# Performance work log

Measured on AMD Instinct MI355X. Metric: run time of the kernel, lower is better.

Reference implementation:

```python
import jax, jax.numpy as jnp
import numpy as np

HEAD_SIZE = 64  # EMBEDDING_SIZE(384) // HEAD_NO(6)

def setup_inputs() -> dict:
    key = jax.random.key(0)
    ks = jax.random.split(key, 6)
    B, T, C, H, D = 256, 256, 384, 6, 64
    s = 0.02
    return {
        "x": jax.random.normal(ks[0], (B, T, C), dtype=jnp.float32),
        "Wq": jax.random.normal(ks[1], (H, C, D), dtype=jnp.float32) * s,
        "Wk": jax.random.normal(ks[2], (H, C, D), dtype=jnp.float32) * s,
        "Wv": jax.random.normal(ks[3], (H, C, D), dtype=jnp.float32) * s,
        "Wproj": jax.random.normal(ks[4], (C, C), dtype=jnp.float32) * s,
        "bproj": jnp.zeros((C,), dtype=jnp.float32),
    }

def reference(x, Wq, Wk, Wv, Wproj, bproj):
    B, T, C = x.shape
    # per-head projections, stacked over heads h: [B, H, T, D]
    q = jnp.einsum('btc,hcd->bhtd', x, Wq)
    k = jnp.einsum('btc,hcd->bhtd', x, Wk)
    v = jnp.einsum('btc,hcd->bhtd', x, Wv)
    scale = 1.0 / jnp.sqrt(jnp.asarray(HEAD_SIZE, dtype=x.dtype))
    # scores [B, H, T, T]; causal mask (masked_fill then /scale == scale then mask, since -inf/scale=-inf)
    scores = jnp.einsum('bhtd,bhsd->bhts', q, k) * scale
    causal = jnp.tril(jnp.ones((T, T), dtype=bool))
    scores = jnp.where(causal, scores, -jnp.inf)
    w = jax.nn.softmax(scores, axis=-1)
    # dropout is identity in eval mode
    out = jnp.einsum('bhts,bhsd->bhtd', w, v)          # [B, H, T, D]
    out = out.transpose(0, 2, 1, 3).reshape(B, T, C)    # concat heads -> [B, T, C]
    return out @ Wproj + bproj
```

## Files before the change

kernel.cpp:

```cpp
#include <hip/hip_runtime.h>
#include <hip/hip_bf16.h>

typedef __bf16 bf16;
typedef unsigned int u32;
typedef __attribute__((ext_vector_type(8))) __bf16 bf16x8;
typedef __attribute__((ext_vector_type(4))) float f32x4;

#define Bsz 256
#define Tsz 256
#define Csz 384
#define Hn  6
#define Dh  64
#define NQKV 1152

#define MFMA16(a, b, c) __builtin_amdgcn_mfma_f32_16x16x32_bf16(a, b, c, 0, 0, 0)

typedef __attribute__((address_space(3))) u32 lds_u32;
typedef __attribute__((address_space(1))) const u32 gbl_u32;
__device__ __forceinline__ void gl2lds16(const void* g, void* l) {
    __builtin_amdgcn_global_load_lds((gbl_u32*)g, (lds_u32*)l, 16, 0, 0);
}

__device__ __forceinline__ float redmax16(float x) {
    x = fmaxf(x, __shfl_xor(x, 1));
    x = fmaxf(x, __shfl_xor(x, 2));
    x = fmaxf(x, __shfl_xor(x, 4));
    x = fmaxf(x, __shfl_xor(x, 8));
    return x;
}
__device__ __forceinline__ float redsum16(float x) {
    x += __shfl_xor(x, 1);
    x += __shfl_xor(x, 2);
    x += __shfl_xor(x, 4);
    x += __shfl_xor(x, 8);
    return x;
}

__global__ __launch_bounds__(256) void convert_x(
    const float* __restrict__ x, bf16* __restrict__ xb)
{
    size_t i = ((size_t)blockIdx.x * 256 + threadIdx.x) * 8;
    float4 f0 = *(const float4*)&x[i];
    float4 f1 = *(const float4*)&x[i + 4];
    bf16x8 o;
    o[0] = (bf16)f0.x; o[1] = (bf16)f0.y; o[2] = (bf16)f0.z; o[3] = (bf16)f0.w;
    o[4] = (bf16)f1.x; o[5] = (bf16)f1.y; o[6] = (bf16)f1.z; o[7] = (bf16)f1.w;
    *(bf16x8*)&xb[i] = o;
}

__global__ __launch_bounds__(384) void prep_w(
    const float* __restrict__ Wq, const float* __restrict__ Wk,
    const float* __restrict__ Wv, const float* __restrict__ Wp,
    bf16* __restrict__ Btqkv, bf16* __restrict__ Bpt)
{
    const int n = blockIdx.x, k = threadIdx.x;
    if (n < NQKV) {
        int wi = n / Csz, rem = n - wi * Csz, h = rem >> 6, d = rem & 63;
        const float* W = wi == 0 ? Wq : (wi == 1 ? Wk : Wv);
        Btqkv[(size_t)n * Csz + k] = (bf16)W[((size_t)h * Csz + k) * Dh + d];
    } else {
        int n2 = n - NQKV;
        Bpt[(size_t)n2 * Csz + k] = (bf16)Wp[(size_t)k * Csz + n2];
    }
}


__device__ __forceinline__ void stage_tile512(
    const char* Ab, const char* Bb, int m0, int n0, int t,
    char* AsB, char* BsB, int tid)
{
    const int srow = tid >> 3;
    const int scs  = ((tid & 7) * 16) ^ ((srow & 7) << 4);
    #pragma unroll
    for (int j = 0; j < 4; ++j)
        gl2lds16(Ab + (size_t)(m0 + j * 64 + srow) * 768 + t * 128 + scs,
                 AsB + j * 8192 + tid * 16);
    #pragma unroll
    for (int j = 0; j < 2; ++j)
        gl2lds16(Bb + (size_t)(n0 + j * 64 + srow) * 768 + t * 128 + scs,
                 BsB + j * 8192 + tid * 16);
}

__device__ __forceinline__ void compute_tile512(
    const char* Ap, const char* Bp,
    int wm4, int wn2, int l4, int quad, f32x4 acc[4][4])
{
    const int cswz = (l4 & 7) << 4;
    bf16x8 bfr[4][2], af[4][2];
    #pragma unroll
    for (int fn = 0; fn < 4; ++fn)
        #pragma unroll
        for (int ks = 0; ks < 2; ++ks)
            bfr[fn][ks] = *(const bf16x8*)(Bp + (wn2 * 64 + fn * 16 + l4) * 128 +
                                           ((ks * 64 + quad * 16) ^ cswz));
    #pragma unroll
    for (int fr = 0; fr < 4; ++fr)
        #pragma unroll
        for (int ks = 0; ks < 2; ++ks)
            af[fr][ks] = *(const bf16x8*)(Ap + (wm4 * 64 + fr * 16 + l4) * 128 +
                                          ((ks * 64 + quad * 16) ^ cswz));
    __builtin_amdgcn_s_setprio(1);
    #pragma unroll
    for (int ks = 0; ks < 2; ++ks)
        #pragma unroll
        for (int fr = 0; fr < 4; ++fr)
            #pragma unroll
            for (int fn = 0; fn < 4; ++fn)
                acc[fr][fn] = MFMA16(af[fr][ks], bfr[fn][ks], acc[fr][fn]);
    __builtin_amdgcn_s_setprio(0);
}

#define GEMM_PIPE8()                                                           \
    stage_tile512(Ab, Bb, m0, n0, 0, As0, Bs0, tid);                           \
    _Pragma("unroll")                                                          \
    for (int t = 0; t < 6; ++t) {                                              \
        if (t < 5) stage_tile512(Ab, Bb, m0, n0, t + 1,                        \
                                 (t & 1) ? As0 : As1, (t & 1) ? Bs0 : Bs1, tid);\
        if (t < 5) { asm volatile("s_waitcnt vmcnt(6)" ::: "memory"); }        \
        else       { asm volatile("s_waitcnt vmcnt(0)" ::: "memory"); }        \
        __builtin_amdgcn_s_barrier();                                          \
        compute_tile512((t & 1) ? As1 : As0, (t & 1) ? Bs1 : Bs0,              \
                        wm4, wn2, l4, quad, acc);                              \
        __builtin_amdgcn_s_barrier();                                          \
    }

__global__ __launch_bounds__(512, 2) void qkv_gemm(
    const bf16* __restrict__ A, const bf16* __restrict__ Bt,
    bf16* __restrict__ q, bf16* __restrict__ k, bf16* __restrict__ v)
{
    __shared__ bf16 As[2][256][64];
    __shared__ bf16 Bs[2][128][64];
    char* As0 = (char*)&As[0][0][0]; char* As1 = (char*)&As[1][0][0];
    char* Bs0 = (char*)&Bs[0][0][0]; char* Bs1 = (char*)&Bs[1][0][0];
    const int tid = threadIdx.x, w = tid >> 6, lane = tid & 63;
    const int l4 = lane & 15, quad = lane >> 4;
    const int wm4 = w >> 1, wn2 = w & 1;

    const int orig = blockIdx.x;
    const int id = (orig & 7) * 288 + (orig >> 3);
    const int mt_ = id / 9, nt_ = id - mt_ * 9;
    const int m0 = mt_ * 256, n0 = nt_ * 128;

    const char* Ab = (const char*)A;
    const char* Bb = (const char*)Bt;
    f32x4 acc[4][4] = {};

    GEMM_PIPE8();

    #pragma unroll
    for (int fn = 0; fn < 4; ++fn) {
        int n = n0 + wn2 * 64 + fn * 16 + l4;
        int wi = n / Csz, rem = n - wi * Csz;
        int h = rem >> 6, d = rem & 63;
        bf16* outp = wi == 0 ? q : (wi == 1 ? k : v);
        #pragma unroll
        for (int fr = 0; fr < 4; ++fr)
            #pragma unroll
            for (int r = 0; r < 4; ++r) {
                int m = m0 + wm4 * 64 + fr * 16 + quad * 4 + r;
                int b = m >> 8, tt = m & 255;
                outp[(((size_t)(b * Hn + h)) * Tsz + tt) * Dh + d] = (bf16)acc[fr][fn][r];
            }
    }
}

__global__ __launch_bounds__(512, 2) void proj_gemm(
    const bf16* __restrict__ A, const bf16* __restrict__ Bt,
    const float* __restrict__ bias, float* __restrict__ out)
{
    __shared__ bf16 As[2][256][64];
    __shared__ bf16 Bs[2][128][64];
    char* As0 = (char*)&As[0][0][0]; char* As1 = (char*)&As[1][0][0];
    char* Bs0 = (char*)&Bs[0][0][0]; char* Bs1 = (char*)&Bs[1][0][0];
    const int tid = threadIdx.x, w = tid >> 6, lane = tid & 63;
    const int l4 = lane & 15, quad = lane >> 4;
    const int wm4 = w >> 1, wn2 = w & 1;

    const int orig = blockIdx.x;
    const int id = (orig & 7) * 96 + (orig >> 3);
    const int mt_ = id / 3, nt_ = id - mt_ * 3;
    const int m0 = mt_ * 256, n0 = nt_ * 128;

    const char* Ab = (const char*)A;
    const char* Bb = (const char*)Bt;
    f32x4 acc[4][4] = {};

    GEMM_PIPE8();

    #pragma unroll
    for (int fn = 0; fn < 4; ++fn) {
        int n = n0 + wn2 * 64 + fn * 16 + l4;
        float bv = bias[n];
        #pragma unroll
        for (int fr = 0; fr < 4; ++fr)
            #pragma unroll
            for (int r = 0; r < 4; ++r) {
                int m = m0 + wm4 * 64 + fr * 16 + quad * 4 + r;
                out[(size_t)m * Csz + n] = acc[fr][fn][r] + bv;
            }
    }
}

__global__ __launch_bounds__(256) void attn_mfma(
    const bf16* __restrict__ q, const bf16* __restrict__ k, const bf16* __restrict__ v,
    bf16* __restrict__ att)
{
    __shared__ bf16 Kl[64][72];
    __shared__ bf16 Vt[64][72];
    __shared__ bf16 Pl[4][16][72];
    const float SCL = 0.18033688f;
    const int tid = threadIdx.x, w = tid >> 6, lane = tid & 63;
    const int l4 = lane & 15, quad = lane >> 4;

    const int orig = blockIdx.x;
    const int blk = (orig & 7) * 768 + (orig >> 3);
    const int bh = blk >> 2, qt = blk & 3;
    const int b = bh / Hn, h = bh % Hn;
    const bf16* qb = q + (size_t)bh * Tsz * Dh;
    const bf16* kb = k + (size_t)bh * Tsz * Dh;
    const bf16* vb = v + (size_t)bh * Tsz * Dh;

    const int trow = qt * 64 + w * 16 + l4;
    const bf16x8 qa0 = *(const bf16x8*)&qb[trow * Dh + quad * 8];
    const bf16x8 qa1 = *(const bf16x8*)&qb[trow * Dh + 32 + quad * 8];

    f32x4 o[4] = {f32x4{0,0,0,0}, f32x4{0,0,0,0}, f32x4{0,0,0,0}, f32x4{0,0,0,0}};
    float mrun[4] = {-3.0e38f, -3.0e38f, -3.0e38f, -3.0e38f};
    float lrun[4] = {0.f, 0.f, 0.f, 0.f};

    for (int kt = 0; kt <= qt; ++kt) {
        #pragma unroll
        for (int it = 0; it < 2; ++it) {
            int idx = it * 256 + tid;
            int s = idx >> 3, d8 = (idx & 7) * 8;
            *(bf16x8*)&Kl[s][d8] = *(const bf16x8*)&kb[(kt * 64 + s) * Dh + d8];
        }
        #pragma unroll
        for (int it = 0; it < 2; ++it) {
            int idx = it * 256 + tid;
            int s = idx & 63, d8 = (idx >> 6) * 8;
            bf16x8 vv = *(const bf16x8*)&vb[(kt * 64 + s) * Dh + d8];
            #pragma unroll
            for (int j = 0; j < 8; ++j) Vt[d8 + j][s] = vv[j];
        }
        __syncthreads();

        f32x4 sc[4] = {f32x4{0,0,0,0}, f32x4{0,0,0,0}, f32x4{0,0,0,0}, f32x4{0,0,0,0}};
        #pragma unroll
        for (int nt = 0; nt < 4; ++nt) {
            bf16x8 b0 = *(const bf16x8*)&Kl[nt * 16 + l4][quad * 8];
            bf16x8 b1 = *(const bf16x8*)&Kl[nt * 16 + l4][32 + quad * 8];
            sc[nt] = MFMA16(qa0, b0, sc[nt]);
            sc[nt] = MFMA16(qa1, b1, sc[nt]);
        }

        float mnew[4], alpha[4];
        #pragma unroll
        for (int r = 0; r < 4; ++r) {
            int tg = qt * 64 + w * 16 + quad * 4 + r;
            float mx = mrun[r];
            #pragma unroll
            for (int nt = 0; nt < 4; ++nt) {
                float sv = sc[nt][r] * SCL;
                int sg = kt * 64 + nt * 16 + l4;
                if (sg > tg) sv = -1.0e30f;
                sc[nt][r] = sv;
                mx = fmaxf(mx, sv);
            }
            mx = redmax16(mx);
            mnew[r] = mx;
            alpha[r] = __builtin_amdgcn_exp2f(mrun[r] - mx);
            mrun[r] = mx;
        }
        #pragma unroll
        for (int r = 0; r < 4; ++r) {
            float sm = 0.f;
            #pragma unroll
            for (int nt = 0; nt < 4; ++nt) {
                float e = __builtin_amdgcn_exp2f(sc[nt][r] - mnew[r]);
                sc[nt][r] = e;
                sm += e;
            }
            sm = redsum16(sm);
            lrun[r] = lrun[r] * alpha[r] + sm;
        }
        #pragma unroll
        for (int nt = 0; nt < 4; ++nt)
            #pragma unroll
            for (int r = 0; r < 4; ++r) o[nt][r] *= alpha[r];

        #pragma unroll
        for (int nt = 0; nt < 4; ++nt)
            #pragma unroll
            for (int r = 0; r < 4; ++r)
                Pl[w][quad * 4 + r][nt * 16 + l4] = (bf16)sc[nt][r];

        bf16x8 pa0 = *(const bf16x8*)&Pl[w][l4][quad * 8];
        bf16x8 pa1 = *(const bf16x8*)&Pl[w][l4][32 + quad * 8];
        #pragma unroll
        for (int nt = 0; nt < 4; ++nt) {
            bf16x8 vb0 = *(const bf16x8*)&Vt[nt * 16 + l4][quad * 8];
            bf16x8 vb1 = *(const bf16x8*)&Vt[nt * 16 + l4][32 + quad * 8];
            o[nt] = MFMA16(pa0, vb0, o[nt]);
            o[nt] = MFMA16(pa1, vb1, o[nt]);
        }
        __syncthreads();
    }

    #pragma unroll
    for (int r = 0; r < 4; ++r) {
        float inv = 1.f / lrun[r];
        int tg = qt * 64 + w * 16 + quad * 4 + r;
        #pragma unroll
        for (int nt = 0; nt < 4; ++nt)
            att[((size_t)(b * Tsz + tg)) * Csz + h * Dh + nt * 16 + l4] =
                (bf16)(o[nt][r] * inv);
    }
}

extern "C" void kernel_launch(void* const* d_in, const int* in_sizes, int n_in,
                              void* d_out, int out_size, void* d_ws, size_t ws_size,
                              hipStream_t stream)
{
    const float* x  = (const float*)d_in[0];
    const float* Wq = (const float*)d_in[1];
    const float* Wk = (const float*)d_in[2];
    const float* Wv = (const float*)d_in[3];
    const float* Wp = (const float*)d_in[4];
    const float* bp = (const float*)d_in[5];
    float* out = (float*)d_out;

    const size_t npe = (size_t)Bsz * Tsz * Csz;
    bf16* xb    = (bf16*)d_ws;
    bf16* att   = xb;
    bf16* q     = xb + npe;
    bf16* k     = q  + npe;
    bf16* v     = k  + npe;
    bf16* Btqkv = v  + npe;
    bf16* Bpt   = Btqkv + (size_t)NQKV * Csz;

    convert_x<<<npe / 2048, 256, 0, stream>>>(x, xb);
    prep_w<<<NQKV + Csz, 384, 0, stream>>>(Wq, Wk, Wv, Wp, Btqkv, Bpt);
    qkv_gemm<<<(Bsz * Tsz / 256) * (NQKV / 128), 512, 0, stream>>>(xb, Btqkv, q, k, v);
    attn_mfma<<<Bsz * Hn * 4, 256, 0, stream>>>(q, k, v, att);
    proj_gemm<<<(Bsz * Tsz / 256) * (Csz / 128), 512, 0, stream>>>(att, Bpt, bp, out);
}
```

Baseline: 388.6 us.

## Restructure attention to one block per (batch, head) with full K/V in LDS

The attention kernel now runs one 512-thread block per (batch, head). It loads all 256 K rows and a transposed V into XOR-swizzled LDS once, so the previous per-query-tile reloads of K/V and the barriers inside the loop are gone. Each wave handles two 16-row query groups chosen as w and 15-w to balance the causal work. Masking is applied only on the diagonal tile, and s_setprio brackets the MFMA sections. The cost is more LDS per block (about 80KB), which limits occupancy, and a smaller grid that may underfill the CUs.

```diff
diff --git a/kernel.cpp b/kernel.cpp
--- a/kernel.cpp
+++ b/kernel.cpp
@@ -201,120 +201,146 @@
     }
 }
 
-__global__ __launch_bounds__(256) void attn_mfma(
+__global__ __launch_bounds__(512, 4) void attn_mfma(
     const bf16* __restrict__ q, const bf16* __restrict__ k, const bf16* __restrict__ v,
     bf16* __restrict__ att)
 {
-    __shared__ bf16 Kl[64][72];
-    __shared__ bf16 Vt[64][72];
-    __shared__ bf16 Pl[4][16][72];
+    __shared__ bf16 Kl[256][64];
+    __shared__ bf16 Vt[64][256];
+    __shared__ bf16 Pl[8][16][64];
     const float SCL = 0.18033688f;
     const int tid = threadIdx.x, w = tid >> 6, lane = tid & 63;
     const int l4 = lane & 15, quad = lane >> 4;
-
-    const int orig = blockIdx.x;
-    const int blk = (orig & 7) * 768 + (orig >> 3);
-    const int bh = blk >> 2, qt = blk & 3;
+    const int cswz = l4 & 7;
+    const int bh = blockIdx.x;
     const int b = bh / Hn, h = bh % Hn;
     const bf16* qb = q + (size_t)bh * Tsz * Dh;
     const bf16* kb = k + (size_t)bh * Tsz * Dh;
     const bf16* vb = v + (size_t)bh * Tsz * Dh;
-
-    const int trow = qt * 64 + w * 16 + l4;
-    const bf16x8 qa0 = *(const bf16x8*)&qb[trow * Dh + quad * 8];
-    const bf16x8 qa1 = *(const bf16x8*)&qb[trow * Dh + 32 + quad * 8];
-
-    f32x4 o[4] = {f32x4{0,0,0,0}, f32x4{0,0,0,0}, f32x4{0,0,0,0}, f32x4{0,0,0,0}};
-    float mrun[4] = {-3.0e38f, -3.0e38f, -3.0e38f, -3.0e38f};
-    float lrun[4] = {0.f, 0.f, 0.f, 0.f};
-
-    for (int kt = 0; kt <= qt; ++kt) {
-        #pragma unroll
-        for (int it = 0; it < 2; ++it) {
-            int idx = it * 256 + tid;
-            int s = idx >> 3, d8 = (idx & 7) * 8;
-            *(bf16x8*)&Kl[s][d8] = *(const bf16x8*)&kb[(kt * 64 + s) * Dh + d8];
+    char* KlB = (char*)&Kl[0][0];
+    char* VtB = (char*)&Vt[0][0];
+    char* PlB = (char*)&Pl[w][0][0];
+
+    bf16x8 qa[2][2];
+    #pragma unroll
+    for (int fi = 0; fi < 2; ++fi) {
+        int g = fi ? 15 - w : w;
+        qa[fi][0] = *(const bf16x8*)&qb[(g * 16 + l4) * Dh + quad * 8];
+        qa[fi][1] = *(const bf16x8*)&qb[(g * 16 + l4) * Dh + 32 + quad * 8];
+    }
+
+    #pragma unroll
+    for (int it = 0; it < 4; ++it) {
+        int c = it * 512 + tid;
+        int row = c >> 3, ck = c & 7;
+        bf16x8 kv = *(const bf16x8*)((const char*)kb + (size_t)c * 16);
+        *(bf16x8*)(KlB + row * 128 + ((ck ^ (row & 7)) << 4)) = kv;
+    }
+    #pragma unroll
+    for (int it = 0; it < 4; ++it) {
+        int idx = it * 512 + tid;
+        int s = idx & 63, g2 = idx >> 6;
+        int d8 = (g2 & 7) * 8, sg = (g2 >> 3) * 64 + s;
+        bf16x8 vv = *(const bf16x8*)&vb[(size_t)sg * Dh + d8];
+        #pragma unroll
+        for (int j = 0; j < 8; ++j) {
+            int row = d8 + j;
+            *(bf16*)(VtB + row * 512 + (((sg >> 3) ^ (row & 7)) << 4) + (sg & 7) * 2) = vv[j];
         }
-        #pragma unroll
-        for (int it = 0; it < 2; ++it) {
-            int idx = it * 256 + tid;
-            int s = idx & 63, d8 = (idx >> 6) * 8;
-            bf16x8 vv = *(const bf16x8*)&vb[(kt * 64 + s) * Dh + d8];
-            #pragma unroll
-            for (int j = 0; j < 8; ++j) Vt[d8 + j][s] = vv[j];
+    }
+    __syncthreads();
+
+    #pragma unroll
+    for (int fi = 0; fi < 2; ++fi) {
+        const int g = fi ? 15 - w : w;
+        const int diag = g >> 2;
+        const int tg = g * 16 + quad * 4;
+        f32x4 o[4] = {f32x4{0,0,0,0}, f32x4{0,0,0,0}, f32x4{0,0,0,0}, f32x4{0,0,0,0}};
+        float mrun[4] = {-3.0e38f, -3.0e38f, -3.0e38f, -3.0e38f};
+        float lrun[4] = {0.f, 0.f, 0.f, 0.f};
+
+        for (int kt = 0; kt <= diag; ++kt) {
+            f32x4 sc[4] = {f32x4{0,0,0,0}, f32x4{0,0,0,0}, f32x4{0,0,0,0}, f32x4{0,0,0,0}};
+            __builtin_amdgcn_s_setprio(1);
+            #pragma unroll
+            for (int nt = 0; nt < 4; ++nt) {
+                const char* kbase = KlB + (kt * 64 + nt * 16 + l4) * 128;
+                bf16x8 b0 = *(const bf16x8*)(kbase + ((quad ^ cswz) << 4));
+                bf16x8 b1 = *(const bf16x8*)(kbase + (((4 + quad) ^ cswz) << 4));
+                sc[nt] = MFMA16(qa[fi][0], b0, sc[nt]);
+                sc[nt] = MFMA16(qa[fi][1], b1, sc[nt]);
+            }
+            __builtin_amdgcn_s_setprio(0);
+
+            const bool isdiag = (kt == diag);
+            float mnew[4], alpha[4];
+            #pragma unroll
+            for (int r = 0; r < 4; ++r) {
+                float mx = mrun[r];
+                #pragma unroll
+                for (int nt = 0; nt < 4; ++nt) {
+                    float sv = sc[nt][r] * SCL;
+                    if (isdiag) {
+                        int sg2 = kt * 64 + nt * 16 + l4;
+                        if (sg2 > tg + r) sv = -1.0e30f;
+                    }
+                    sc[nt][r] = sv;
+                    mx = fmaxf(mx, sv);
+                }
+                mx = redmax16(mx);
+                mnew[r] = mx;
+                alpha[r] = __builtin_amdgcn_exp2f(mrun[r] - mx);
+                mrun[r] = mx;
+            }
+            #pragma unroll
+            for (int r = 0; r < 4; ++r) {
+                float sm = 0.f;
+                #pragma unroll
+                for (int nt = 0; nt < 4; ++nt) {
+                    float e = __builtin_amdgcn_exp2f(sc[nt][r] - mnew[r]);
+                    sc[nt][r] = e;
+                    sm += e;
+                }
+                sm = redsum16(sm);
+                lrun[r] = lrun[r] * alpha[r] + sm;
+            }
+            #pragma unroll
+            for (int nt = 0; nt < 4; ++nt)
+                #pragma unroll
+                for (int r = 0; r < 4; ++r) o[nt][r] *= alpha[r];
+
+            #pragma unroll
+            for (int nt = 0; nt < 4; ++nt)
+                #pragma unroll
+                for (int r = 0; r < 4; ++r) {
+                    int row = quad * 4 + r;
+                    int colc = nt * 2 + (l4 >> 3);
+                    *(bf16*)(PlB + row * 128 + ((colc ^ (row & 7)) << 4) + (l4 & 7) * 2)
+                        = (bf16)sc[nt][r];
+                }
+            bf16x8 pa0 = *(const bf16x8*)(PlB + l4 * 128 + ((quad ^ cswz) << 4));
+            bf16x8 pa1 = *(const bf16x8*)(PlB + l4 * 128 + (((4 + quad) ^ cswz) << 4));
+
+            __builtin_amdgcn_s_setprio(1);
+            #pragma unroll
+            for (int nt = 0; nt < 4; ++nt) {
+                const char* vbase = VtB + (nt * 16 + l4) * 512;
+                bf16x8 v0 = *(const bf16x8*)(vbase + (((kt * 8 + quad) ^ cswz) << 4));
+                bf16x8 v1 = *(const bf16x8*)(vbase + (((kt * 8 + 4 + quad) ^ cswz) << 4));
+                o[nt] = MFMA16(pa0, v0, o[nt]);
+                o[nt] = MFMA16(pa1, v1, o[nt]);
+            }
+            __builtin_amdgcn_s_setprio(0);
         }
-        __syncthreads();
-
-        f32x4 sc[4] = {f32x4{0,0,0,0}, f32x4{0,0,0,0}, f32x4{0,0,0,0}, f32x4{0,0,0,0}};
-        #pragma unroll
-        for (int nt = 0; nt < 4; ++nt) {
-            bf16x8 b0 = *(const bf16x8*)&Kl[nt * 16 + l4][quad * 8];
-            bf16x8 b1 = *(const bf16x8*)&Kl[nt * 16 + l4][32 + quad * 8];
-            sc[nt] = MFMA16(qa0, b0, sc[nt]);
-            sc[nt] = MFMA16(qa1, b1, sc[nt]);
+
+        #pragma unroll
+        for (int r = 0; r < 4; ++r) {
+            float inv = 1.f / lrun[r];
+            #pragma unroll
+            for (int nt = 0; nt < 4; ++nt)
+                att[((size_t)(b * Tsz + tg + r)) * Csz + h * Dh + nt * 16 + l4] =
+                    (bf16)(o[nt][r] * inv);
         }
-
-        float mnew[4], alpha[4];
-        #pragma unroll
-        for (int r = 0; r < 4; ++r) {
-            int tg = qt * 64 + w * 16 + quad * 4 + r;
-            float mx = mrun[r];
-            #pragma unroll
-            for (int nt = 0; nt < 4; ++nt) {
-                float sv = sc[nt][r] * SCL;
-                int sg = kt * 64 + nt * 16 + l4;
-                if (sg > tg) sv = -1.0e30f;
-                sc[nt][r] = sv;
-                mx = fmaxf(mx, sv);
-            }
-            mx = redmax16(mx);
-            mnew[r] = mx;
-            alpha[r] = __builtin_amdgcn_exp2f(mrun[r] - mx);
-            mrun[r] = mx;
-        }
-        #pragma unroll
-        for (int r = 0; r < 4; ++r) {
-            float sm = 0.f;
-            #pragma unroll
-            for (int nt = 0; nt < 4; ++nt) {
-                float e = __builtin_amdgcn_exp2f(sc[nt][r] - mnew[r]);
-                sc[nt][r] = e;
-                sm += e;
-            }
-            sm = redsum16(sm);
-            lrun[r] = lrun[r] * alpha[r] + sm;
-        }
-        #pragma unroll
-        for (int nt = 0; nt < 4; ++nt)
-            #pragma unroll
-            for (int r = 0; r < 4; ++r) o[nt][r] *= alpha[r];
-
-        #pragma unroll
-        for (int nt = 0; nt < 4; ++nt)
-            #pragma unroll
-            for (int r = 0; r < 4; ++r)
-                Pl[w][quad * 4 + r][nt * 16 + l4] = (bf16)sc[nt][r];
-
-        bf16x8 pa0 = *(const bf16x8*)&Pl[w][l4][quad * 8];
-        bf16x8 pa1 = *(const bf16x8*)&Pl[w][l4][32 + quad * 8];
-        #pragma unroll
-        for (int nt = 0; nt < 4; ++nt) {
-            bf16x8 vb0 = *(const bf16x8*)&Vt[nt * 16 + l4][quad * 8];
-            bf16x8 vb1 = *(const bf16x8*)&Vt[nt * 16 + l4][32 + quad * 8];
-            o[nt] = MFMA16(pa0, vb0, o[nt]);
-            o[nt] = MFMA16(pa1, vb1, o[nt]);
-        }
-        __syncthreads();
-    }
-
-    #pragma unroll
-    for (int r = 0; r < 4; ++r) {
-        float inv = 1.f / lrun[r];
-        int tg = qt * 64 + w * 16 + quad * 4 + r;
-        #pragma unroll
-        for (int nt = 0; nt < 4; ++nt)
-            att[((size_t)(b * Tsz + tg)) * Csz + h * Dh + nt * 16 + l4] =
-                (bf16)(o[nt][r] * inv);
     }
 }
 
@@ -342,6 +368,6 @@
     convert_x<<<npe / 2048, 256, 0, stream>>>(x, xb);
     prep_w<<<NQKV + Csz, 384, 0, stream>>>(Wq, Wk, Wv, Wp, Btqkv, Bpt);
     qkv_gemm<<<(Bsz * Tsz / 256) * (NQKV / 128), 512, 0, stream>>>(xb, Btqkv, q, k, v);
-    attn_mfma<<<Bsz * Hn * 4, 256, 0, stream>>>(q, k, v, att);
+    attn_mfma<<<Bsz * Hn, 512, 0, stream>>>(q, k, v, att);
     proj_gemm<<<(Bsz * Tsz / 256) * (Csz / 128), 512, 0, stream>>>(att, Bpt, bp, out);
 }
```

After: 369.6 us. 4.9% less time.
